# Kernel optimization log

Hardware: AMD Instinct MI355X
Metric: run time of the kernel (lower is better)

## Reference

```python
import jax, jax.numpy as jnp
import numpy as np

N = 8192
F_IN, HID, LAT = 256, 128, 32


def setup_inputs() -> dict:
    key = jax.random.key(0)
    k1, k2, k3, k4 = jax.random.split(key, 4)
    X = jax.random.normal(k1, (N, F_IN), dtype=jnp.float32)
    # Dense normalized-adjacency stand-in (original converts dense A_tilde to COO each call)
    A_tilde = jax.random.uniform(k2, (N, N), dtype=jnp.float32) / N
    # Xavier-uniform init like torch's init.xavier_uniform_ on Linear weights
    lim1 = float(np.sqrt(6.0 / (F_IN + HID)))
    lim2 = float(np.sqrt(6.0 / (HID + LAT)))
    W1 = jax.random.uniform(k3, (F_IN, HID), dtype=jnp.float32, minval=-lim1, maxval=lim1)
    W2 = jax.random.uniform(k4, (HID, LAT), dtype=jnp.float32, minval=-lim2, maxval=lim2)
    return {"X": X, "A_tilde": A_tilde, "W1": W1, "W2": W2}


def reference(X, A_tilde, W1, W2):
    # GCN layer 1: A_tilde @ (X W1), then ReLU
    h = jax.nn.relu(A_tilde @ (X @ W1))          # [N, HID]
    # GCN layer 2 (no activation)
    Z = A_tilde @ (h @ W2)                        # [N, LAT]
    # Inner-product decoder
    A_hat = jax.nn.sigmoid(Z @ Z.T)               # [N, N]
    return A_hat
```

## Files before the change

### kernel.cpp

```cpp
#include <hip/hip_runtime.h>
#include <hip/hip_bf16.h>

#define N_ 8192
#define F_ 256
#define H_ 128
#define L_ 32
#define TK 64
#define KQN 4
#define KQL (N_ / KQN)

typedef __attribute__((ext_vector_type(8))) short bf16x8;
typedef __attribute__((ext_vector_type(4))) float f32x4;
typedef __attribute__((ext_vector_type(4))) short bf16x4;

__device__ __forceinline__ unsigned f2bf_u(float x) {
    unsigned u = __builtin_bit_cast(unsigned, x);
    return (u + 0x7fffu + ((u >> 16) & 1u)) >> 16;
}
__device__ __forceinline__ short f2bf(float x) { return (short)f2bf_u(x); }

__device__ __forceinline__ bf16x4 cvt4(float4 a) {
    bf16x4 v;
    v[0] = f2bf(a.x); v[1] = f2bf(a.y); v[2] = f2bf(a.z); v[3] = f2bf(a.w);
    return v;
}
__device__ __forceinline__ bf16x8 cvt8(float4 a, float4 b) {
    bf16x8 v;
    v[0] = f2bf(a.x); v[1] = f2bf(a.y); v[2] = f2bf(a.z); v[3] = f2bf(a.w);
    v[4] = f2bf(b.x); v[5] = f2bf(b.y); v[6] = f2bf(b.z); v[7] = f2bf(b.w);
    return v;
}

__global__ __launch_bounds__(256) void k1_xw1(const float* __restrict__ X,
                                              const float* __restrict__ W1,
                                              short* __restrict__ XW1T) {
    __shared__ short w1t[H_ * (F_ + 8)];
    const int tid = threadIdx.x;
    for (int idx = tid; idx < F_ * H_; idx += 256) {
        int k = idx >> 7, n = idx & 127;
        w1t[n * (F_ + 8) + k] = f2bf(W1[idx]);
    }
    __syncthreads();
    const int wv = tid >> 6, l = tid & 63;
    const int lm = l & 15, q = l >> 4;
    const int i0 = blockIdx.x * 64 + wv * 16;
    const float* xrow = X + (size_t)(i0 + lm) * F_;
    f32x4 acc[8];
#pragma unroll
    for (int j = 0; j < 8; ++j) acc[j] = (f32x4){0.f, 0.f, 0.f, 0.f};
#pragma unroll
    for (int k0 = 0; k0 < F_; k0 += 32) {
        float4 a0 = *(const float4*)(xrow + k0 + q * 8);
        float4 a1 = *(const float4*)(xrow + k0 + q * 8 + 4);
        bf16x8 af = cvt8(a0, a1);
#pragma unroll
        for (int j = 0; j < 8; ++j) {
            bf16x8 bf = *(const bf16x8*)&w1t[(j * 16 + lm) * (F_ + 8) + k0 + q * 8];
            acc[j] = __builtin_amdgcn_mfma_f32_16x16x32_bf16(af, bf, acc[j], 0, 0, 0);
        }
    }
#pragma unroll
    for (int j = 0; j < 8; ++j) {
        bf16x4 o;
        o[0] = f2bf(acc[j][0]); o[1] = f2bf(acc[j][1]);
        o[2] = f2bf(acc[j][2]); o[3] = f2bf(acc[j][3]);
        *(bf16x4*)(XW1T + (size_t)(j * 16 + lm) * N_ + i0 + q * 4) = o;
    }
}

__global__ __launch_bounds__(512) void k2a(const float* __restrict__ A,
                                           const short* __restrict__ XW1T,
                                           float* __restrict__ P4) {
    __shared__ short As[2][64][72];
    __shared__ short Bs[2][128][72];
    const int tid = threadIdx.x;
    const int bi = blockIdx.x >> 2, kq = blockIdx.x & 3;
    const int i0 = bi * 64, kbase = kq * KQL;
    const int ar = tid >> 4, ac = (tid & 15) * 4;
    const int br = tid >> 3, bc = (tid & 7) * 8;
    const float* Ap = A + (size_t)(i0 + ar) * N_ + kbase + ac;
    const short* Bp = XW1T + (size_t)br * N_ + kbase + bc;

    const int wv = tid >> 6, l = tid & 63, lm = l & 15, q = l >> 4;
    const int rg = wv & 3, ch = wv >> 2;

    float4 pa0, pa1; bf16x8 pb0, pb1;
#define LOADG(s) do { size_t o = (size_t)(s) * TK; \
        pa0 = *(const float4*)(Ap + o); \
        pa1 = *(const float4*)(Ap + o + (size_t)32 * N_); \
        pb0 = *(const bf16x8*)(Bp + o); \
        pb1 = *(const bf16x8*)(Bp + o + (size_t)64 * N_); } while (0)
#define STORES(b) do { \
        *(bf16x4*)&As[b][ar][ac] = cvt4(pa0); \
        *(bf16x4*)&As[b][ar + 32][ac] = cvt4(pa1); \
        *(bf16x8*)&Bs[b][br][bc] = pb0; \
        *(bf16x8*)&Bs[b][br + 64][bc] = pb1; } while (0)

    LOADG(0); STORES(0); LOADG(1);
    __syncthreads();

    f32x4 acc[4];
#pragma unroll
    for (int j = 0; j < 4; ++j) acc[j] = (f32x4){0.f, 0.f, 0.f, 0.f};
    const int NS = KQL / TK;
#pragma unroll 2
    for (int s = 0; s < NS; ++s) {
        const int b = s & 1;
#pragma unroll
        for (int kh = 0; kh < 2; ++kh) {
            bf16x8 af = *(const bf16x8*)&As[b][rg * 16 + lm][kh * 32 + q * 8];
#pragma unroll
            for (int jt = 0; jt < 4; ++jt) {
                bf16x8 bfv = *(const bf16x8*)&Bs[b][ch * 64 + jt * 16 + lm][kh * 32 + q * 8];
                acc[jt] = __builtin_amdgcn_mfma_f32_16x16x32_bf16(af, bfv, acc[jt], 0, 0, 0);
            }
        }
        if (s + 1 < NS) {
            STORES((s + 1) & 1);
            if (s + 2 < NS) LOADG(s + 2);
        }
        __syncthreads();
    }
#undef LOADG
#undef STORES
    float* Pb = P4 + ((size_t)kq * N_ + i0 + rg * 16 + q * 4) * H_ + ch * 64 + lm;
#pragma unroll
    for (int jt = 0; jt < 4; ++jt)
#pragma unroll
        for (int r = 0; r < 4; ++r)
            Pb[(size_t)r * H_ + jt * 16] = acc[jt][r];
}

__global__ __launch_bounds__(256) void k2b(const float* __restrict__ P4,
                                           const float* __restrict__ W2,
                                           short* __restrict__ ZPT) {
    __shared__ short hl[32][136];
    __shared__ short w2t[32][136];
    const int tid = threadIdx.x;
    for (int idx = tid; idx < H_ * L_; idx += 256) {
        int k = idx >> 5, j = idx & 31;
        w2t[j][k] = f2bf(W2[idx]);
    }
    const int i0 = blockIdx.x * 32;
    const int r = tid >> 3, c16 = (tid & 7) * 16;
    float4 v[4];
#pragma unroll
    for (int cc = 0; cc < 4; ++cc) v[cc] = (float4){0.f, 0.f, 0.f, 0.f};
#pragma unroll
    for (int kq = 0; kq < 4; ++kq) {
        const float* p = P4 + ((size_t)kq * N_ + i0 + r) * H_ + c16;
#pragma unroll
        for (int cc = 0; cc < 4; ++cc) {
            float4 t = *(const float4*)(p + cc * 4);
            v[cc].x += t.x; v[cc].y += t.y; v[cc].z += t.z; v[cc].w += t.w;
        }
    }
#pragma unroll
    for (int cc = 0; cc < 4; ++cc) {
        v[cc].x = v[cc].x > 0.f ? v[cc].x : 0.f;
        v[cc].y = v[cc].y > 0.f ? v[cc].y : 0.f;
        v[cc].z = v[cc].z > 0.f ? v[cc].z : 0.f;
        v[cc].w = v[cc].w > 0.f ? v[cc].w : 0.f;
    }
    *(bf16x8*)&hl[r][c16] = cvt8(v[0], v[1]);
    *(bf16x8*)&hl[r][c16 + 8] = cvt8(v[2], v[3]);
    __syncthreads();
    const int wv = tid >> 6, l = tid & 63, lm = l & 15, q = l >> 4;
    const int ti = wv & 1, tj = wv >> 1;
    f32x4 a2 = (f32x4){0.f, 0.f, 0.f, 0.f};
#pragma unroll
    for (int k0 = 0; k0 < H_; k0 += 32) {
        bf16x8 af = *(const bf16x8*)&hl[ti * 16 + lm][k0 + q * 8];
        bf16x8 bf = *(const bf16x8*)&w2t[tj * 16 + lm][k0 + q * 8];
        a2 = __builtin_amdgcn_mfma_f32_16x16x32_bf16(af, bf, a2, 0, 0, 0);
    }
    bf16x4 o;
    o[0] = f2bf(a2[0]); o[1] = f2bf(a2[1]); o[2] = f2bf(a2[2]); o[3] = f2bf(a2[3]);
    *(bf16x4*)(ZPT + (size_t)(tj * 16 + lm) * N_ + i0 + ti * 16 + q * 4) = o;
}

__global__ __launch_bounds__(512) void k3a(const float* __restrict__ A,
                                           const short* __restrict__ ZPT,
                                           float* __restrict__ Q4) {
    __shared__ short As[2][64][72];
    __shared__ short Bs[2][32][72];
    const int tid = threadIdx.x;
    const int bi = blockIdx.x >> 2, kq = blockIdx.x & 3;
    const int i0 = bi * 64, kbase = kq * KQL;
    const int ar = tid >> 4, ac = (tid & 15) * 4;
    const int br = tid >> 4, bc = (tid & 15) * 4;
    const float* Ap = A + (size_t)(i0 + ar) * N_ + kbase + ac;
    const short* Bp = ZPT + (size_t)br * N_ + kbase + bc;

    const int wv = tid >> 6, l = tid & 63, lm = l & 15, q = l >> 4;
    const int rg = wv & 3, ch = wv >> 2;

    float4 pa0, pa1; bf16x4 pb0;
#define LOADG(s) do { size_t o = (size_t)(s) * TK; \
        pa0 = *(const float4*)(Ap + o); \
        pa1 = *(const float4*)(Ap + o + (size_t)32 * N_); \
        pb0 = *(const bf16x4*)(Bp + o); } while (0)
#define STORES(b) do { \
        *(bf16x4*)&As[b][ar][ac] = cvt4(pa0); \
        *(bf16x4*)&As[b][ar + 32][ac] = cvt4(pa1); \
        *(bf16x4*)&Bs[b][br][bc] = pb0; } while (0)

    LOADG(0); STORES(0); LOADG(1);
    __syncthreads();

    f32x4 acc = (f32x4){0.f, 0.f, 0.f, 0.f};
    const int NS = KQL / TK;
#pragma unroll 2
    for (int s = 0; s < NS; ++s) {
        const int b = s & 1;
#pragma unroll
        for (int kh = 0; kh < 2; ++kh) {
            bf16x8 af = *(const bf16x8*)&As[b][rg * 16 + lm][kh * 32 + q * 8];
            bf16x8 bfv = *(const bf16x8*)&Bs[b][ch * 16 + lm][kh * 32 + q * 8];
            acc = __builtin_amdgcn_mfma_f32_16x16x32_bf16(af, bfv, acc, 0, 0, 0);
        }
        if (s + 1 < NS) {
            STORES((s + 1) & 1);
            if (s + 2 < NS) LOADG(s + 2);
        }
        __syncthreads();
    }
#undef LOADG
#undef STORES
    float* Qb = Q4 + ((size_t)kq * N_ + i0 + rg * 16 + q * 4) * L_ + ch * 16 + lm;
#pragma unroll
    for (int r = 0; r < 4; ++r)
        Qb[(size_t)r * L_] = acc[r];
}

__global__ __launch_bounds__(256) void k3b(const float* __restrict__ Q4,
                                           short* __restrict__ Z) {
    size_t g = ((size_t)blockIdx.x * 256 + threadIdx.x) * 8;
    float4 s0 = (float4){0.f, 0.f, 0.f, 0.f}, s1 = s0;
#pragma unroll
    for (int kq = 0; kq < 4; ++kq) {
        const float* p = Q4 + (size_t)kq * N_ * L_ + g;
        float4 a = *(const float4*)(p);
        float4 b = *(const float4*)(p + 4);
        s0.x += a.x; s0.y += a.y; s0.z += a.z; s0.w += a.w;
        s1.x += b.x; s1.y += b.y; s1.z += b.z; s1.w += b.w;
    }
    *(bf16x8*)(Z + g) = cvt8(s0, s1);
}

__global__ __launch_bounds__(256) void k4_dec(const short* __restrict__ Z,
                                              float* __restrict__ out) {
    __shared__ float os[128][132];
    const int tid = threadIdx.x;
    const int wv = tid >> 6, l = tid & 63;
    const int lm = l & 15, q = l >> 4;
    const int bj = blockIdx.x & 63, bi = blockIdx.x >> 6;
    const int i0 = bi * 128, j0 = bj * 128;
    bf16x8 af[2];
#pragma unroll
    for (int t = 0; t < 2; ++t)
        af[t] = *(const bf16x8*)(Z + (size_t)(i0 + wv * 32 + t * 16 + lm) * L_ + q * 8);
#pragma unroll
    for (int tj = 0; tj < 8; ++tj) {
        bf16x8 bfv = *(const bf16x8*)(Z + (size_t)(j0 + tj * 16 + lm) * L_ + q * 8);
#pragma unroll
        for (int t = 0; t < 2; ++t) {
            f32x4 c = __builtin_amdgcn_mfma_f32_16x16x32_bf16(
                af[t], bfv, (f32x4){0.f, 0.f, 0.f, 0.f}, 0, 0, 0);
#pragma unroll
            for (int r = 0; r < 4; ++r) {
                float e = __expf(-c[r]);
                os[wv * 32 + t * 16 + q * 4 + r][tj * 16 + lm] = __fdividef(1.f, 1.f + e);
            }
        }
    }
    __syncthreads();
    for (int idx = tid; idx < 128 * 32; idx += 256) {
        int row = idx >> 5, c4 = idx & 31;
        *(float4*)(out + (size_t)(i0 + row) * N_ + j0 + c4 * 4) = *(const float4*)&os[row][c4 * 4];
    }
}

extern "C" void kernel_launch(void* const* d_in, const int* in_sizes, int n_in,
                              void* d_out, int out_size, void* d_ws, size_t ws_size,
                              hipStream_t stream) {
    const float* X  = (const float*)d_in[0];
    const float* A  = (const float*)d_in[1];
    const float* W1 = (const float*)d_in[2];
    const float* W2 = (const float*)d_in[3];
    float* out = (float*)d_out;

    short* XW1T = (short*)d_ws;
    short* ZPT  = XW1T + (size_t)H_ * N_;
    short* Z    = ZPT + (size_t)L_ * N_;
    float* P4   = (float*)(Z + (size_t)N_ * L_);
    float* Q4   = P4 + (size_t)4 * N_ * H_;

    k1_xw1<<<N_ / 64, 256, 0, stream>>>(X, W1, XW1T);
    k2a<<<(N_ / 64) * KQN, 512, 0, stream>>>(A, XW1T, P4);
    k2b<<<N_ / 32, 256, 0, stream>>>(P4, W2, ZPT);
    k3a<<<(N_ / 64) * KQN, 512, 0, stream>>>(A, ZPT, Q4);
    k3b<<<(N_ * L_) / (256 * 8), 256, 0, stream>>>(Q4, Z);
    k4_dec<<<(N_ / 128) * (N_ / 128), 256, 0, stream>>>(Z, out);
}
```

Measured before the change: 560.4 us.

## Stash bf16 copy of A in first pass, reuse it in second GEMM

The first A-GEMM now also writes its bf16-converted A tile to a workspace buffer, and the second A-GEMM reads that half-size copy instead of re-reading and re-converting the fp32 adjacency. The layer-1 loop is manually unrolled by two with separate prefetch register sets, and the decoder kernel uses 64-row tiles with a fully unrolled store loop. The extra bf16 write costs bandwidth in the first pass, and the path depends on the workspace being large enough for a 128MB buffer, falling back to the old kernel otherwise.

```diff
diff --git a/kernel.cpp b/kernel.cpp
--- a/kernel.cpp
+++ b/kernel.cpp
@@ -68,9 +68,11 @@
     }
 }
 
+template <int WRITE_AB>
 __global__ __launch_bounds__(512) void k2a(const float* __restrict__ A,
                                            const short* __restrict__ XW1T,
-                                           float* __restrict__ P4) {
+                                           float* __restrict__ P4,
+                                           short* __restrict__ Ab) {
     __shared__ short As[2][64][72];
     __shared__ short Bs[2][128][72];
     const int tid = threadIdx.x;
@@ -80,49 +82,56 @@
     const int br = tid >> 3, bc = (tid & 7) * 8;
     const float* Ap = A + (size_t)(i0 + ar) * N_ + kbase + ac;
     const short* Bp = XW1T + (size_t)br * N_ + kbase + bc;
+    short* Abp = Ab + (size_t)(i0 + ar) * N_ + kbase + ac;
 
     const int wv = tid >> 6, l = tid & 63, lm = l & 15, q = l >> 4;
     const int rg = wv & 3, ch = wv >> 2;
 
-    float4 pa0, pa1; bf16x8 pb0, pb1;
-#define LOADG(s) do { size_t o = (size_t)(s) * TK; \
-        pa0 = *(const float4*)(Ap + o); \
-        pa1 = *(const float4*)(Ap + o + (size_t)32 * N_); \
-        pb0 = *(const bf16x8*)(Bp + o); \
-        pb1 = *(const bf16x8*)(Bp + o + (size_t)64 * N_); } while (0)
-#define STORES(b) do { \
-        *(bf16x4*)&As[b][ar][ac] = cvt4(pa0); \
-        *(bf16x4*)&As[b][ar + 32][ac] = cvt4(pa1); \
-        *(bf16x8*)&Bs[b][br][bc] = pb0; \
-        *(bf16x8*)&Bs[b][br + 64][bc] = pb1; } while (0)
-
-    LOADG(0); STORES(0); LOADG(1);
+    float4 Pa0, Pa1; bf16x8 Pb0, Pb1;
+    float4 Qa0, Qa1; bf16x8 Qb0, Qb1;
+
+#define LOADG2(S, o_) do { size_t _o = (size_t)(o_) * TK; \
+        S##a0 = *(const float4*)(Ap + _o); \
+        S##a1 = *(const float4*)(Ap + _o + (size_t)32 * N_); \
+        S##b0 = *(const bf16x8*)(Bp + _o); \
+        S##b1 = *(const bf16x8*)(Bp + _o + (size_t)64 * N_); } while (0)
+#define STORES2(S, b_, o_) do { \
+        bf16x4 _c0 = cvt4(S##a0), _c1 = cvt4(S##a1); \
+        *(bf16x4*)&As[b_][ar][ac] = _c0; \
+        *(bf16x4*)&As[b_][ar + 32][ac] = _c1; \
+        *(bf16x8*)&Bs[b_][br][bc] = S##b0; \
+        *(bf16x8*)&Bs[b_][br + 64][bc] = S##b1; \
+        if (WRITE_AB) { size_t _o = (size_t)(o_) * TK; \
+            *(bf16x4*)(Abp + _o) = _c0; \
+            *(bf16x4*)(Abp + _o + (size_t)32 * N_) = _c1; } } while (0)
+#define MFMAPH2(b_) do { \
+        for (int kh = 0; kh < 2; ++kh) { \
+            bf16x8 af = *(const bf16x8*)&As[b_][rg * 16 + lm][kh * 32 + q * 8]; \
+            for (int jt = 0; jt < 4; ++jt) { \
+                bf16x8 bfv = *(const bf16x8*)&Bs[b_][ch * 64 + jt * 16 + lm][kh * 32 + q * 8]; \
+                acc[jt] = __builtin_amdgcn_mfma_f32_16x16x32_bf16(af, bfv, acc[jt], 0, 0, 0); \
+            } } } while (0)
+
+    LOADG2(P, 0); STORES2(P, 0, 0); LOADG2(Q, 1);
     __syncthreads();
 
     f32x4 acc[4];
 #pragma unroll
     for (int j = 0; j < 4; ++j) acc[j] = (f32x4){0.f, 0.f, 0.f, 0.f};
     const int NS = KQL / TK;
-#pragma unroll 2
-    for (int s = 0; s < NS; ++s) {
-        const int b = s & 1;
-#pragma unroll
-        for (int kh = 0; kh < 2; ++kh) {
-            bf16x8 af = *(const bf16x8*)&As[b][rg * 16 + lm][kh * 32 + q * 8];
-#pragma unroll
-            for (int jt = 0; jt < 4; ++jt) {
-                bf16x8 bfv = *(const bf16x8*)&Bs[b][ch * 64 + jt * 16 + lm][kh * 32 + q * 8];
-                acc[jt] = __builtin_amdgcn_mfma_f32_16x16x32_bf16(af, bfv, acc[jt], 0, 0, 0);
-            }
-        }
-        if (s + 1 < NS) {
-            STORES((s + 1) & 1);
-            if (s + 2 < NS) LOADG(s + 2);
-        }
-        __syncthreads();
-    }
-#undef LOADG
-#undef STORES
+    for (int s = 0; s < NS; s += 2) {
+        if (s + 2 < NS) LOADG2(P, s + 2);
+        MFMAPH2(0);
+        STORES2(Q, 1, s + 1);
+        __syncthreads();
+        if (s + 3 < NS) LOADG2(Q, s + 3);
+        MFMAPH2(1);
+        if (s + 2 < NS) STORES2(P, 0, s + 2);
+        __syncthreads();
+    }
+#undef LOADG2
+#undef STORES2
+#undef MFMAPH2
     float* Pb = P4 + ((size_t)kq * N_ + i0 + rg * 16 + q * 4) * H_ + ch * 64 + lm;
 #pragma unroll
     for (int jt = 0; jt < 4; ++jt)
@@ -179,9 +188,65 @@
     *(bf16x4*)(ZPT + (size_t)(tj * 16 + lm) * N_ + i0 + ti * 16 + q * 4) = o;
 }
 
-__global__ __launch_bounds__(512) void k3a(const float* __restrict__ A,
-                                           const short* __restrict__ ZPT,
-                                           float* __restrict__ Q4) {
+__global__ __launch_bounds__(512) void k3a_bf(const short* __restrict__ Ab,
+                                              const short* __restrict__ ZPT,
+                                              float* __restrict__ Q4) {
+    __shared__ short As[2][64][72];
+    __shared__ short Bs[2][32][72];
+    const int tid = threadIdx.x;
+    const int bi = blockIdx.x >> 2, kq = blockIdx.x & 3;
+    const int i0 = bi * 64, kbase = kq * KQL;
+    const int ar8 = tid >> 3, ac8 = (tid & 7) * 8;
+    const int br = tid >> 4, bc = (tid & 15) * 4;
+    const short* Ap = Ab + (size_t)(i0 + ar8) * N_ + kbase + ac8;
+    const short* Bp = ZPT + (size_t)br * N_ + kbase + bc;
+
+    const int wv = tid >> 6, l = tid & 63, lm = l & 15, q = l >> 4;
+    const int rg = wv & 3, ch = wv >> 2;
+
+    bf16x8 Pa; bf16x4 Pb;
+    bf16x8 Qa; bf16x4 Qb;
+
+#define LOADG3(S, o_) do { size_t _o = (size_t)(o_) * TK; \
+        S##a = *(const bf16x8*)(Ap + _o); \
+        S##b = *(const bf16x4*)(Bp + _o); } while (0)
+#define STORES3(S, b_) do { \
+        *(bf16x8*)&As[b_][ar8][ac8] = S##a; \
+        *(bf16x4*)&Bs[b_][br][bc] = S##b; } while (0)
+#define MFMAPH3(b_) do { \
+        for (int kh = 0; kh < 2; ++kh) { \
+            bf16x8 af = *(const bf16x8*)&As[b_][rg * 16 + lm][kh * 32 + q * 8]; \
+            bf16x8 bfv = *(const bf16x8*)&Bs[b_][ch * 16 + lm][kh * 32 + q * 8]; \
+            acc = __builtin_amdgcn_mfma_f32_16x16x32_bf16(af, bfv, acc, 0, 0, 0); \
+        } } while (0)
+
+    LOADG3(P, 0); STORES3(P, 0); LOADG3(Q, 1);
+    __syncthreads();
+
+    f32x4 acc = (f32x4){0.f, 0.f, 0.f, 0.f};
+    const int NS = KQL / TK;
+    for (int s = 0; s < NS; s += 2) {
+        if (s + 2 < NS) LOADG3(P, s + 2);
+        MFMAPH3(0);
+        STORES3(Q, 1);
+        __syncthreads();
+        if (s + 3 < NS) LOADG3(Q, s + 3);
+        MFMAPH3(1);
+        if (s + 2 < NS) STORES3(P, 0);
+        __syncthreads();
+    }
+#undef LOADG3
+#undef STORES3
+#undef MFMAPH3
+    float* Qb_ = Q4 + ((size_t)kq * N_ + i0 + rg * 16 + q * 4) * L_ + ch * 16 + lm;
+#pragma unroll
+    for (int r = 0; r < 4; ++r)
+        Qb_[(size_t)r * L_] = acc[r];
+}
+
+__global__ __launch_bounds__(512) void k3a_f32(const float* __restrict__ A,
+                                               const short* __restrict__ ZPT,
+                                               float* __restrict__ Q4) {
     __shared__ short As[2][64][72];
     __shared__ short Bs[2][32][72];
     const int tid = threadIdx.x;
@@ -196,16 +261,16 @@
     const int rg = wv & 3, ch = wv >> 2;
 
     float4 pa0, pa1; bf16x4 pb0;
-#define LOADG(s) do { size_t o = (size_t)(s) * TK; \
+#define LOADG0(s) do { size_t o = (size_t)(s) * TK; \
         pa0 = *(const float4*)(Ap + o); \
         pa1 = *(const float4*)(Ap + o + (size_t)32 * N_); \
         pb0 = *(const bf16x4*)(Bp + o); } while (0)
-#define STORES(b) do { \
+#define STORES0(b) do { \
         *(bf16x4*)&As[b][ar][ac] = cvt4(pa0); \
         *(bf16x4*)&As[b][ar + 32][ac] = cvt4(pa1); \
         *(bf16x4*)&Bs[b][br][bc] = pb0; } while (0)
 
-    LOADG(0); STORES(0); LOADG(1);
+    LOADG0(0); STORES0(0); LOADG0(1);
     __syncthreads();
 
     f32x4 acc = (f32x4){0.f, 0.f, 0.f, 0.f};
@@ -220,13 +285,13 @@
             acc = __builtin_amdgcn_mfma_f32_16x16x32_bf16(af, bfv, acc, 0, 0, 0);
         }
         if (s + 1 < NS) {
-            STORES((s + 1) & 1);
-            if (s + 2 < NS) LOADG(s + 2);
-        }
-        __syncthreads();
-    }
-#undef LOADG
-#undef STORES
+            STORES0((s + 1) & 1);
+            if (s + 2 < NS) LOADG0(s + 2);
+        }
+        __syncthreads();
+    }
+#undef LOADG0
+#undef STORES0
     float* Qb = Q4 + ((size_t)kq * N_ + i0 + rg * 16 + q * 4) * L_ + ch * 16 + lm;
 #pragma unroll
     for (int r = 0; r < 4; ++r)
@@ -250,32 +315,28 @@
 
 __global__ __launch_bounds__(256) void k4_dec(const short* __restrict__ Z,
                                               float* __restrict__ out) {
-    __shared__ float os[128][132];
+    __shared__ float os[64][132];
     const int tid = threadIdx.x;
     const int wv = tid >> 6, l = tid & 63;
     const int lm = l & 15, q = l >> 4;
     const int bj = blockIdx.x & 63, bi = blockIdx.x >> 6;
-    const int i0 = bi * 128, j0 = bj * 128;
-    bf16x8 af[2];
-#pragma unroll
-    for (int t = 0; t < 2; ++t)
-        af[t] = *(const bf16x8*)(Z + (size_t)(i0 + wv * 32 + t * 16 + lm) * L_ + q * 8);
+    const int i0 = bi * 64, j0 = bj * 128;
+    bf16x8 af = *(const bf16x8*)(Z + (size_t)(i0 + wv * 16 + lm) * L_ + q * 8);
 #pragma unroll
     for (int tj = 0; tj < 8; ++tj) {
         bf16x8 bfv = *(const bf16x8*)(Z + (size_t)(j0 + tj * 16 + lm) * L_ + q * 8);
-#pragma unroll
-        for (int t = 0; t < 2; ++t) {
-            f32x4 c = __builtin_amdgcn_mfma_f32_16x16x32_bf16(
-                af[t], bfv, (f32x4){0.f, 0.f, 0.f, 0.f}, 0, 0, 0);
-#pragma unroll
-            for (int r = 0; r < 4; ++r) {
-                float e = __expf(-c[r]);
-                os[wv * 32 + t * 16 + q * 4 + r][tj * 16 + lm] = __fdividef(1.f, 1.f + e);
-            }
-        }
-    }
-    __syncthreads();
-    for (int idx = tid; idx < 128 * 32; idx += 256) {
+        f32x4 c = __builtin_amdgcn_mfma_f32_16x16x32_bf16(
+            af, bfv, (f32x4){0.f, 0.f, 0.f, 0.f}, 0, 0, 0);
+#pragma unroll
+        for (int r = 0; r < 4; ++r) {
+            float e = __expf(-c[r]);
+            os[wv * 16 + q * 4 + r][tj * 16 + lm] = __fdividef(1.f, 1.f + e);
+        }
+    }
+    __syncthreads();
+#pragma unroll
+    for (int it = 0; it < 8; ++it) {
+        int idx = it * 256 + tid;
         int row = idx >> 5, c4 = idx & 31;
         *(float4*)(out + (size_t)(i0 + row) * N_ + j0 + c4 * 4) = *(const float4*)&os[row][c4 * 4];
     }
@@ -295,11 +356,22 @@
     short* Z    = ZPT + (size_t)L_ * N_;
     float* P4   = (float*)(Z + (size_t)N_ * L_);
     float* Q4   = P4 + (size_t)4 * N_ * H_;
+    short* Ab   = (short*)(Q4 + (size_t)4 * N_ * L_);
+
+    size_t base = ((size_t)H_ * N_ + (size_t)L_ * N_ + (size_t)N_ * L_) * sizeof(short)
+                + ((size_t)4 * N_ * H_ + (size_t)4 * N_ * L_) * sizeof(float);
+    bool useAb = ws_size >= base + (size_t)N_ * N_ * sizeof(short);
 
     k1_xw1<<<N_ / 64, 256, 0, stream>>>(X, W1, XW1T);
-    k2a<<<(N_ / 64) * KQN, 512, 0, stream>>>(A, XW1T, P4);
+    if (useAb)
+        k2a<1><<<(N_ / 64) * KQN, 512, 0, stream>>>(A, XW1T, P4, Ab);
+    else
+        k2a<0><<<(N_ / 64) * KQN, 512, 0, stream>>>(A, XW1T, P4, Ab);
     k2b<<<N_ / 32, 256, 0, stream>>>(P4, W2, ZPT);
-    k3a<<<(N_ / 64) * KQN, 512, 0, stream>>>(A, ZPT, Q4);
+    if (useAb)
+        k3a_bf<<<(N_ / 64) * KQN, 512, 0, stream>>>(Ab, ZPT, Q4);
+    else
+        k3a_f32<<<(N_ / 64) * KQN, 512, 0, stream>>>(A, ZPT, Q4);
     k3b<<<(N_ * L_) / (256 * 8), 256, 0, stream>>>(Q4, Z);
-    k4_dec<<<(N_ / 128) * (N_ / 128), 256, 0, stream>>>(Z, out);
-}
+    k4_dec<<<(N_ / 64) * (N_ / 128), 256, 0, stream>>>(Z, out);
+}
```

Result: no change. 552.7 us (-1.4%).

## Cache bf16 copy of adjacency in k2a and reuse it in second propagation

Applied to the files above, without the earlier changes.

The first A-propagation kernel now reads A straight from global memory into registers, with no shared-memory staging. When the workspace is large enough, it also writes a bf16 copy of A. The second propagation kernel then streams that bf16 copy, which halves its A read traffic; otherwise it falls back to a direct-load fp32 kernel. The block index order is swapped so blocks sharing a K-quarter run together, and the decoder tile is shrunk to 64 rows. In exchange, k2a gains an extra 128 MB write, and dropping LDS staging means redundant global B loads across waves.

```diff
diff --git a/kernel.cpp b/kernel.cpp
--- a/kernel.cpp
+++ b/kernel.cpp
@@ -5,7 +5,6 @@
 #define F_ 256
 #define H_ 128
 #define L_ 32
-#define TK 64
 #define KQN 4
 #define KQL (N_ / KQN)
 
@@ -68,61 +67,37 @@
     }
 }
 
-__global__ __launch_bounds__(512) void k2a(const float* __restrict__ A,
-                                           const short* __restrict__ XW1T,
-                                           float* __restrict__ P4) {
-    __shared__ short As[2][64][72];
-    __shared__ short Bs[2][128][72];
-    const int tid = threadIdx.x;
-    const int bi = blockIdx.x >> 2, kq = blockIdx.x & 3;
+template <int WRITE_AB>
+__global__ __launch_bounds__(512, 6) void k2a(const float* __restrict__ A,
+                                              const short* __restrict__ XW1T,
+                                              float* __restrict__ P4,
+                                              short* __restrict__ Ab) {
+    const int tid = threadIdx.x;
+    const int bi = blockIdx.x & 127, kq = blockIdx.x >> 7;
     const int i0 = bi * 64, kbase = kq * KQL;
-    const int ar = tid >> 4, ac = (tid & 15) * 4;
-    const int br = tid >> 3, bc = (tid & 7) * 8;
-    const float* Ap = A + (size_t)(i0 + ar) * N_ + kbase + ac;
-    const short* Bp = XW1T + (size_t)br * N_ + kbase + bc;
-
     const int wv = tid >> 6, l = tid & 63, lm = l & 15, q = l >> 4;
     const int rg = wv & 3, ch = wv >> 2;
 
-    float4 pa0, pa1; bf16x8 pb0, pb1;
-#define LOADG(s) do { size_t o = (size_t)(s) * TK; \
-        pa0 = *(const float4*)(Ap + o); \
-        pa1 = *(const float4*)(Ap + o + (size_t)32 * N_); \
-        pb0 = *(const bf16x8*)(Bp + o); \
-        pb1 = *(const bf16x8*)(Bp + o + (size_t)64 * N_); } while (0)
-#define STORES(b) do { \
-        *(bf16x4*)&As[b][ar][ac] = cvt4(pa0); \
-        *(bf16x4*)&As[b][ar + 32][ac] = cvt4(pa1); \
-        *(bf16x8*)&Bs[b][br][bc] = pb0; \
-        *(bf16x8*)&Bs[b][br + 64][bc] = pb1; } while (0)
-
-    LOADG(0); STORES(0); LOADG(1);
-    __syncthreads();
+    const float* Arow = A + (size_t)(i0 + rg * 16 + lm) * N_ + kbase + q * 8;
+    short* Abrow = Ab + (size_t)(i0 + rg * 16 + lm) * N_ + kbase + q * 8;
+    const short* B0 = XW1T + (size_t)(ch * 64 + lm) * N_ + kbase + q * 8;
 
     f32x4 acc[4];
 #pragma unroll
     for (int j = 0; j < 4; ++j) acc[j] = (f32x4){0.f, 0.f, 0.f, 0.f};
-    const int NS = KQL / TK;
+
 #pragma unroll 2
-    for (int s = 0; s < NS; ++s) {
-        const int b = s & 1;
-#pragma unroll
-        for (int kh = 0; kh < 2; ++kh) {
-            bf16x8 af = *(const bf16x8*)&As[b][rg * 16 + lm][kh * 32 + q * 8];
-#pragma unroll
-            for (int jt = 0; jt < 4; ++jt) {
-                bf16x8 bfv = *(const bf16x8*)&Bs[b][ch * 64 + jt * 16 + lm][kh * 32 + q * 8];
-                acc[jt] = __builtin_amdgcn_mfma_f32_16x16x32_bf16(af, bfv, acc[jt], 0, 0, 0);
-            }
-        }
-        if (s + 1 < NS) {
-            STORES((s + 1) & 1);
-            if (s + 2 < NS) LOADG(s + 2);
-        }
-        __syncthreads();
-    }
-#undef LOADG
-#undef STORES
+    for (int k = 0; k < KQL; k += 32) {
+        float4 a0 = *(const float4*)(Arow + k);
+        float4 a1 = *(const float4*)(Arow + k + 4);
+        bf16x8 af = cvt8(a0, a1);
+        if (WRITE_AB && ch == 0) *(bf16x8*)(Abrow + k) = af;
+#pragma unroll
+        for (int jt = 0; jt < 4; ++jt) {
+            bf16x8 bfv = *(const bf16x8*)(B0 + (size_t)jt * 16 * N_ + k);
+            acc[jt] = __builtin_amdgcn_mfma_f32_16x16x32_bf16(af, bfv, acc[jt], 0, 0, 0);
+        }
+    }
     float* Pb = P4 + ((size_t)kq * N_ + i0 + rg * 16 + q * 4) * H_ + ch * 64 + lm;
 #pragma unroll
     for (int jt = 0; jt < 4; ++jt)
@@ -179,54 +154,52 @@
     *(bf16x4*)(ZPT + (size_t)(tj * 16 + lm) * N_ + i0 + ti * 16 + q * 4) = o;
 }
 
-__global__ __launch_bounds__(512) void k3a(const float* __restrict__ A,
-                                           const short* __restrict__ ZPT,
-                                           float* __restrict__ Q4) {
-    __shared__ short As[2][64][72];
-    __shared__ short Bs[2][32][72];
-    const int tid = threadIdx.x;
-    const int bi = blockIdx.x >> 2, kq = blockIdx.x & 3;
+__global__ __launch_bounds__(512, 8) void k3a_bf(const short* __restrict__ Ab,
+                                                 const short* __restrict__ ZPT,
+                                                 float* __restrict__ Q4) {
+    const int tid = threadIdx.x;
+    const int bi = blockIdx.x & 127, kq = blockIdx.x >> 7;
     const int i0 = bi * 64, kbase = kq * KQL;
-    const int ar = tid >> 4, ac = (tid & 15) * 4;
-    const int br = tid >> 4, bc = (tid & 15) * 4;
-    const float* Ap = A + (size_t)(i0 + ar) * N_ + kbase + ac;
-    const short* Bp = ZPT + (size_t)br * N_ + kbase + bc;
-
     const int wv = tid >> 6, l = tid & 63, lm = l & 15, q = l >> 4;
     const int rg = wv & 3, ch = wv >> 2;
 
-    float4 pa0, pa1; bf16x4 pb0;
-#define LOADG(s) do { size_t o = (size_t)(s) * TK; \
-        pa0 = *(const float4*)(Ap + o); \
-        pa1 = *(const float4*)(Ap + o + (size_t)32 * N_); \
-        pb0 = *(const bf16x4*)(Bp + o); } while (0)
-#define STORES(b) do { \
-        *(bf16x4*)&As[b][ar][ac] = cvt4(pa0); \
-        *(bf16x4*)&As[b][ar + 32][ac] = cvt4(pa1); \
-        *(bf16x4*)&Bs[b][br][bc] = pb0; } while (0)
-
-    LOADG(0); STORES(0); LOADG(1);
-    __syncthreads();
+    const short* Arow = Ab + (size_t)(i0 + rg * 16 + lm) * N_ + kbase + q * 8;
+    const short* Brow = ZPT + (size_t)(ch * 16 + lm) * N_ + kbase + q * 8;
 
     f32x4 acc = (f32x4){0.f, 0.f, 0.f, 0.f};
-    const int NS = KQL / TK;
+#pragma unroll 4
+    for (int k = 0; k < KQL; k += 32) {
+        bf16x8 af = *(const bf16x8*)(Arow + k);
+        bf16x8 bfv = *(const bf16x8*)(Brow + k);
+        acc = __builtin_amdgcn_mfma_f32_16x16x32_bf16(af, bfv, acc, 0, 0, 0);
+    }
+    float* Qb_ = Q4 + ((size_t)kq * N_ + i0 + rg * 16 + q * 4) * L_ + ch * 16 + lm;
+#pragma unroll
+    for (int r = 0; r < 4; ++r)
+        Qb_[(size_t)r * L_] = acc[r];
+}
+
+__global__ __launch_bounds__(512, 6) void k3a_f32(const float* __restrict__ A,
+                                                  const short* __restrict__ ZPT,
+                                                  float* __restrict__ Q4) {
+    const int tid = threadIdx.x;
+    const int bi = blockIdx.x & 127, kq = blockIdx.x >> 7;
+    const int i0 = bi * 64, kbase = kq * KQL;
+    const int wv = tid >> 6, l = tid & 63, lm = l & 15, q = l >> 4;
+    const int rg = wv & 3, ch = wv >> 2;
+
+    const float* Arow = A + (size_t)(i0 + rg * 16 + lm) * N_ + kbase + q * 8;
+    const short* Brow = ZPT + (size_t)(ch * 16 + lm) * N_ + kbase + q * 8;
+
+    f32x4 acc = (f32x4){0.f, 0.f, 0.f, 0.f};
 #pragma unroll 2
-    for (int s = 0; s < NS; ++s) {
-        const int b = s & 1;
-#pragma unroll
-        for (int kh = 0; kh < 2; ++kh) {
-            bf16x8 af = *(const bf16x8*)&As[b][rg * 16 + lm][kh * 32 + q * 8];
-            bf16x8 bfv = *(const bf16x8*)&Bs[b][ch * 16 + lm][kh * 32 + q * 8];
-            acc = __builtin_amdgcn_mfma_f32_16x16x32_bf16(af, bfv, acc, 0, 0, 0);
-        }
-        if (s + 1 < NS) {
-            STORES((s + 1) & 1);
-            if (s + 2 < NS) LOADG(s + 2);
-        }
-        __syncthreads();
-    }
-#undef LOADG
-#undef STORES
+    for (int k = 0; k < KQL; k += 32) {
+        float4 a0 = *(const float4*)(Arow + k);
+        float4 a1 = *(const float4*)(Arow + k + 4);
+        bf16x8 af = cvt8(a0, a1);
+        bf16x8 bfv = *(const bf16x8*)(Brow + k);
+        acc = __builtin_amdgcn_mfma_f32_16x16x32_bf16(af, bfv, acc, 0, 0, 0);
+    }
     float* Qb = Q4 + ((size_t)kq * N_ + i0 + rg * 16 + q * 4) * L_ + ch * 16 + lm;
 #pragma unroll
     for (int r = 0; r < 4; ++r)
@@ -250,32 +223,28 @@
 
 __global__ __launch_bounds__(256) void k4_dec(const short* __restrict__ Z,
                                               float* __restrict__ out) {
-    __shared__ float os[128][132];
+    __shared__ float os[64][132];
     const int tid = threadIdx.x;
     const int wv = tid >> 6, l = tid & 63;
     const int lm = l & 15, q = l >> 4;
     const int bj = blockIdx.x & 63, bi = blockIdx.x >> 6;
-    const int i0 = bi * 128, j0 = bj * 128;
-    bf16x8 af[2];
-#pragma unroll
-    for (int t = 0; t < 2; ++t)
-        af[t] = *(const bf16x8*)(Z + (size_t)(i0 + wv * 32 + t * 16 + lm) * L_ + q * 8);
+    const int i0 = bi * 64, j0 = bj * 128;
+    bf16x8 af = *(const bf16x8*)(Z + (size_t)(i0 + wv * 16 + lm) * L_ + q * 8);
 #pragma unroll
     for (int tj = 0; tj < 8; ++tj) {
         bf16x8 bfv = *(const bf16x8*)(Z + (size_t)(j0 + tj * 16 + lm) * L_ + q * 8);
-#pragma unroll
-        for (int t = 0; t < 2; ++t) {
-            f32x4 c = __builtin_amdgcn_mfma_f32_16x16x32_bf16(
-                af[t], bfv, (f32x4){0.f, 0.f, 0.f, 0.f}, 0, 0, 0);
-#pragma unroll
-            for (int r = 0; r < 4; ++r) {
-                float e = __expf(-c[r]);
-                os[wv * 32 + t * 16 + q * 4 + r][tj * 16 + lm] = __fdividef(1.f, 1.f + e);
-            }
+        f32x4 c = __builtin_amdgcn_mfma_f32_16x16x32_bf16(
+            af, bfv, (f32x4){0.f, 0.f, 0.f, 0.f}, 0, 0, 0);
+#pragma unroll
+        for (int r = 0; r < 4; ++r) {
+            float e = __expf(-c[r]);
+            os[wv * 16 + q * 4 + r][tj * 16 + lm] = __fdividef(1.f, 1.f + e);
         }
     }
     __syncthreads();
-    for (int idx = tid; idx < 128 * 32; idx += 256) {
+#pragma unroll
+    for (int it = 0; it < 8; ++it) {
+        int idx = it * 256 + tid;
         int row = idx >> 5, c4 = idx & 31;
         *(float4*)(out + (size_t)(i0 + row) * N_ + j0 + c4 * 4) = *(const float4*)&os[row][c4 * 4];
     }
@@ -295,11 +264,22 @@
     short* Z    = ZPT + (size_t)L_ * N_;
     float* P4   = (float*)(Z + (size_t)N_ * L_);
     float* Q4   = P4 + (size_t)4 * N_ * H_;
+    short* Ab   = (short*)(Q4 + (size_t)4 * N_ * L_);
+
+    size_t base = ((size_t)H_ * N_ + (size_t)L_ * N_ + (size_t)N_ * L_) * sizeof(short)
+                + ((size_t)4 * N_ * H_ + (size_t)4 * N_ * L_) * sizeof(float);
+    bool useAb = ws_size >= base + (size_t)N_ * N_ * sizeof(short);
 
     k1_xw1<<<N_ / 64, 256, 0, stream>>>(X, W1, XW1T);
-    k2a<<<(N_ / 64) * KQN, 512, 0, stream>>>(A, XW1T, P4);
+    if (useAb)
+        k2a<1><<<(N_ / 64) * KQN, 512, 0, stream>>>(A, XW1T, P4, Ab);
+    else
+        k2a<0><<<(N_ / 64) * KQN, 512, 0, stream>>>(A, XW1T, P4, Ab);
     k2b<<<N_ / 32, 256, 0, stream>>>(P4, W2, ZPT);
-    k3a<<<(N_ / 64) * KQN, 512, 0, stream>>>(A, ZPT, Q4);
+    if (useAb)
+        k3a_bf<<<(N_ / 64) * KQN, 512, 0, stream>>>(Ab, ZPT, Q4);
+    else
+        k3a_f32<<<(N_ / 64) * KQN, 512, 0, stream>>>(A, ZPT, Q4);
     k3b<<<(N_ * L_) / (256 * 8), 256, 0, stream>>>(Q4, Z);
-    k4_dec<<<(N_ / 128) * (N_ / 128), 256, 0, stream>>>(Z, out);
-}
+    k4_dec<<<(N_ / 64) * (N_ / 128), 256, 0, stream>>>(Z, out);
+}
```

Result: slower. 728.2 us (+29.9%).
